# Performance work log

Measured on AMD Instinct MI355X. Metric: run time of the kernel, lower is better.

The kernel has to match this reference:

```python
import jax, jax.numpy as jnp
import numpy as np


def _lstm_layer(x, W, U, b):
    """Keras-style LSTM (gate order i,f,c,o). x: (B,T,F). Returns (hs: (B,T,H), h_last: (B,H))."""
    B, T, F = x.shape
    H = U.shape[0]
    # Precompute input projections for all timesteps: (T, B, 4H)
    zx = jnp.einsum('btf,fk->tbk', x, W) + b

    def step(carry, zx_t):
        h, c = carry
        z = zx_t + h @ U  # (B, 4H)
        i, f, g, o = jnp.split(z, 4, axis=-1)
        i = jax.nn.sigmoid(i)
        f = jax.nn.sigmoid(f)
        g = jnp.tanh(g)
        o = jax.nn.sigmoid(o)
        c = f * c + i * g
        h = o * jnp.tanh(c)
        return (h, c), h

    h0 = jnp.zeros((B, H), dtype=x.dtype)
    c0 = jnp.zeros((B, H), dtype=x.dtype)
    (h_last, _), hs = jax.lax.scan(step, (h0, c0), zx)
    return jnp.transpose(hs, (1, 0, 2)), h_last


def setup_inputs() -> dict:
    key = jax.random.key(0)
    ks = jax.random.split(key, 8)
    B, T, F, H, L = 512, 128, 64, 1024, 1
    s = 0.05
    return {
        'x': jax.random.normal(ks[0], (B, T, F), dtype=jnp.float32),
        'W1': jax.random.normal(ks[1], (F, 4 * H), dtype=jnp.float32) * s,
        'U1': jax.random.normal(ks[2], (H, 4 * H), dtype=jnp.float32) * s,
        'b1': jnp.zeros((4 * H,), dtype=jnp.float32),
        'W2': jax.random.normal(ks[3], (H, 4 * H), dtype=jnp.float32) * s,
        'U2': jax.random.normal(ks[4], (H, 4 * H), dtype=jnp.float32) * s,
        'b2': jnp.zeros((4 * H,), dtype=jnp.float32),
        'Wd': jax.random.normal(ks[5], (H, L), dtype=jnp.float32) * s,
        'bd': jnp.zeros((L,), dtype=jnp.float32),
    }


def reference(x, W1, U1, b1, W2, U2, b2, Wd, bd):
    # Layer 1: return_sequences=True (dropout inactive at inference)
    h1_seq, _ = _lstm_layer(x, W1, U1, b1)
    # Layer 2: return_sequences=False -> last hidden state
    _, h2_last = _lstm_layer(h1_seq, W2, U2, b2)
    # Dense sigmoid head
    return jax.nn.sigmoid(h2_last @ Wd + bd)
```

## Files before the change

kernel.cpp:

```cpp
#include <hip/hip_runtime.h>
#include <hip/hip_bf16.h>
#include <cstdint>


typedef __attribute__((ext_vector_type(8))) _Float16 half8;
typedef __attribute__((ext_vector_type(4))) float    float4v;

__device__ __forceinline__ float sigf(float x) { return 1.0f / (1.0f + __expf(-x)); }
__device__ __forceinline__ float tanhfast(float x) { return 2.0f * sigf(2.0f * x) - 1.0f; }

static constexpr size_t HPS = 32ull * 32 * 512;

struct FragSet {
    half8 A[4];
    half8 B[4][2];
};

__global__ __launch_bounds__(512, 2) void fused_step(
    int s,
    const _Float16* __restrict__ xp,
    const _Float16* __restrict__ P1,
    const _Float16* __restrict__ P2,
    const float* __restrict__ b1, float* __restrict__ c1, _Float16* __restrict__ h1p,
    const float* __restrict__ b2, float* __restrict__ c2, _Float16* __restrict__ h2p)
{
    const int b    = blockIdx.x;
    const int role = (b >> 3) & 1;
    const int tile = ((b >> 4) << 3) | (b & 7);

    const _Float16 *As0, *As1, *Pk;
    const float* bias; float* cs; _Float16* hop;
    int KC0, KCB, KCT;
    if (role == 0) {
        const int t = s; if (t >= 128) return;
        As0 = xp + (size_t)t * 32768;  KC0 = 2;
        As1 = h1p + (size_t)(t & 1) * HPS;
        Pk = P1; KCB = 34; KCT = 34;
        bias = b1; cs = c1;
        hop = h1p + (size_t)(1 - (t & 1)) * HPS;
    } else {
        const int t = s - 1; if (t < 0) return;
        As0 = h1p + (size_t)(1 - (t & 1)) * HPS; KC0 = 32;
        As1 = h2p + (size_t)(t & 1) * HPS;
        Pk = P2; KCB = 64; KCT = 64;
        bias = b2; cs = c2;
        hop = h2p + (size_t)(1 - (t & 1)) * HPS;
    }

    const int tid = threadIdx.x;
    const int w   = tid >> 6;
    const int l   = tid & 63;
    const int q   = l >> 4;
    const int c16 = l & 15;
    const int mh  = w & 1;
    const int kp  = w >> 1;

    const int m0  = (tile >> 5) * 128;
    const int n0  = (tile & 31) * 32;
    const int mG0 = (m0 >> 4) + mh * 4;

    const size_t l8 = (size_t)l * 8;

    const _Float16* bp[4][2];
#pragma unroll
    for (int g = 0; g < 4; ++g)
#pragma unroll
        for (int nf = 0; nf < 2; ++nf)
            bp[g][nf] = Pk + ((size_t)(g * 64 + (n0 >> 4) + nf) * KCB) * 512 + l8;

    float4v acc[4][4][2] = {};

    auto loadS = [&](int kc, FragSet& S) {
        const _Float16* ab; size_t astr;
        if (kc < KC0) { ab = As0 + (size_t)kc * 512;         astr = (size_t)KC0 * 512; }
        else          { ab = As1 + (size_t)(kc - KC0) * 512; astr = 32ull * 512; }
        ab += (size_t)mG0 * astr + l8;
#pragma unroll
        for (int ms = 0; ms < 4; ++ms)
            S.A[ms] = *(const half8*)(ab + (size_t)ms * astr);
#pragma unroll
        for (int g = 0; g < 4; ++g)
#pragma unroll
            for (int nf = 0; nf < 2; ++nf)
                S.B[g][nf] = *(const half8*)(bp[g][nf] + (size_t)kc * 512);
    };
    auto computeS = [&](const FragSet& S) {
#pragma unroll
        for (int g = 0; g < 4; ++g)
#pragma unroll
            for (int ms = 0; ms < 4; ++ms)
#pragma unroll
                for (int nf = 0; nf < 2; ++nf)
                    acc[g][ms][nf] = __builtin_amdgcn_mfma_f32_16x16x32_f16(
                        S.A[ms], S.B[g][nf], acc[g][ms][nf], 0, 0, 0);
    };

    const int base = KCT >> 2;
    const int rem  = KCT & 3;
    const int len  = base + (kp < rem ? 1 : 0);
    const int kcS  = kp * base + (kp < rem ? kp : rem);

    FragSet S;
#pragma unroll 2
    for (int kc = kcS; kc < kcS + len; ++kc) {
        loadS(kc, S);
        computeS(S);
    }

    __shared__ float4v red[8][16][64];
    if ((kp & 1) == 0) {
#pragma unroll
        for (int g = 0; g < 4; ++g)
#pragma unroll
            for (int ms = 0; ms < 4; ++ms)
                red[w][g * 4 + ms][l] = acc[g][ms][1];
    } else {
#pragma unroll
        for (int g = 0; g < 4; ++g)
#pragma unroll
            for (int ms = 0; ms < 4; ++ms)
                red[w][g * 4 + ms][l] = acc[g][ms][0];
    }
    __syncthreads();
    float4v acc1[4][4];
    if ((kp & 1) == 0) {
#pragma unroll
        for (int g = 0; g < 4; ++g)
#pragma unroll
            for (int ms = 0; ms < 4; ++ms)
                acc1[g][ms] = acc[g][ms][0] + red[w ^ 2][g * 4 + ms][l];
    } else {
#pragma unroll
        for (int g = 0; g < 4; ++g)
#pragma unroll
            for (int ms = 0; ms < 4; ++ms)
                acc1[g][ms] = acc[g][ms][1] + red[w ^ 2][g * 4 + ms][l];
    }
    __syncthreads();
    if ((kp >> 1) == 0) {
#pragma unroll
        for (int g = 0; g < 4; ++g)
#pragma unroll
            for (int j = 0; j < 2; ++j)
                red[w][g * 2 + j][l] = acc1[g][2 + j];
    } else {
#pragma unroll
        for (int g = 0; g < 4; ++g)
#pragma unroll
            for (int j = 0; j < 2; ++j)
                red[w][g * 2 + j][l] = acc1[g][j];
    }
    __syncthreads();
    float4v out[4][2];
    if ((kp >> 1) == 0) {
#pragma unroll
        for (int g = 0; g < 4; ++g)
#pragma unroll
            for (int j = 0; j < 2; ++j)
                out[g][j] = acc1[g][j] + red[w ^ 4][g * 2 + j][l];
    } else {
#pragma unroll
        for (int g = 0; g < 4; ++g)
#pragma unroll
            for (int j = 0; j < 2; ++j)
                out[g][j] = acc1[g][2 + j] + red[w ^ 4][g * 2 + j][l];
    }

    const int own_nf  = kp & 1;
    const int own_msp = kp >> 1;
    const int ng = n0 + own_nf * 16 + c16;
    const float bi  = bias[ng];
    const float bff = bias[1024 + ng];
    const float bg  = bias[2048 + ng];
    const float bo  = bias[3072 + ng];
    const int kcH   = n0 >> 5;
    const int laneW = (own_nf * 2 + (c16 >> 3)) << 4;
    const int jW    = c16 & 7;
    float4v* cfrag = (float4v*)cs;
    const size_t cbase = ((size_t)tile * 8 + w) * 2;
#pragma unroll
    for (int j = 0; j < 2; ++j) {
        const int msg = own_msp * 2 + j;
        const int mG  = mG0 + msg;
        _Float16* hg = hop + ((size_t)(mG * 32 + kcH)) * 512 + (size_t)laneW * 8 + jW;
        float4v cold = cfrag[(cbase + j) * 64 + l];
        float4v cnew;
#pragma unroll
        for (int i = 0; i < 4; ++i) {
            const float zi = out[0][j][i] + bi;
            const float zf = out[1][j][i] + bff;
            const float zg = out[2][j][i] + bg;
            const float zo = out[3][j][i] + bo;
            const float ig = sigf(zi);
            const float fg = sigf(zf);
            const float gg = tanhfast(zg);
            const float og = sigf(zo);
            const float cc = fg * cold[i] + ig * gg;
            cnew[i] = cc;
            hg[(q * 4 + i) * 8] = (_Float16)(og * tanhfast(cc));
        }
        cfrag[(cbase + j) * 64 + l] = cnew;
    }
}

__global__ void pack_weights(const float* __restrict__ W, const float* __restrict__ U,
                             int KA, int KC, _Float16* __restrict__ out)
{
    const size_t e = (size_t)blockIdx.x * blockDim.x + threadIdx.x;
    const size_t total = (size_t)256 * KC * 512;
    if (e >= total) return;
    const int j    = (int)(e & 7);
    const int lane = (int)((e >> 3) & 63);
    const size_t g = e >> 9;
    const int kc  = (int)(g % KC);
    const int ntG = (int)(g / KC);
    const int col = ntG * 16 + (lane & 15);
    const int k   = kc * 32 + (lane >> 4) * 8 + j;
    const float v = (k < KA) ? W[(size_t)k * 4096 + col]
                             : U[(size_t)(k - KA) * 4096 + col];
    out[e] = (_Float16)v;
}

__global__ void pack_x(const float* __restrict__ x, _Float16* __restrict__ xp)
{
    const int e = blockIdx.x * blockDim.x + threadIdx.x;
    if (e >= 512 * 128 * 64) return;
    const int j  = e & 7;
    const int l  = (e >> 3) & 63;
    const int g  = e >> 9;
    const int kc = g & 1;
    const int tm = g >> 1;
    const int mG = tm & 31;
    const int t  = tm >> 5;
    const int m  = mG * 16 + (l & 15);
    const int f  = kc * 32 + (l >> 4) * 8 + j;
    xp[e] = (_Float16)x[((size_t)m * 128 + t) * 64 + f];
}

__global__ __launch_bounds__(64) void dense_head(const _Float16* __restrict__ h2p,
                                                 const float* __restrict__ Wd,
                                                 const float* __restrict__ bd,
                                                 float* __restrict__ out)
{
    const int mG = blockIdx.x;
    const int l  = threadIdx.x;
    float s = 0.0f;
    for (int kc = 0; kc < 32; ++kc) {
        half8 f = *(const half8*)(h2p + ((size_t)(mG * 32 + kc)) * 512 + (size_t)l * 8);
        const int kb = kc * 32 + (l >> 4) * 8;
#pragma unroll
        for (int j = 0; j < 8; ++j) s += (float)f[j] * Wd[kb + j];
    }
    s += __shfl_xor(s, 16);
    s += __shfl_xor(s, 32);
    if (l < 16) out[mG * 16 + l] = 1.0f / (1.0f + __expf(-(s + bd[0])));
}


extern "C" void kernel_launch(void* const* d_in, const int* in_sizes, int n_in,
                              void* d_out, int out_size, void* d_ws, size_t ws_size,
                              hipStream_t stream)
{
    const float* x  = (const float*)d_in[0];
    const float* W1 = (const float*)d_in[1];
    const float* U1 = (const float*)d_in[2];
    const float* b1 = (const float*)d_in[3];
    const float* W2 = (const float*)d_in[4];
    const float* U2 = (const float*)d_in[5];
    const float* b2 = (const float*)d_in[6];
    const float* Wd = (const float*)d_in[7];
    const float* bd = (const float*)d_in[8];
    float* out = (float*)d_out;

    char* ws = (char*)d_ws;
    size_t off = 0;
    auto alloc = [&](size_t bytes) {
        char* p = ws + off;
        off = (off + bytes + 255) & ~(size_t)255;
        return p;
    };
    _Float16* xp  = (_Float16*)alloc(512ull * 128 * 64 * 2);
    _Float16* P1  = (_Float16*)alloc(256ull * 34 * 512 * 2);
    _Float16* P2  = (_Float16*)alloc(256ull * 64 * 512 * 2);
    _Float16* h1p = (_Float16*)alloc(2ull * HPS * 2);
    _Float16* h2p = (_Float16*)alloc(2ull * HPS * 2);
    float*    c1  = (float*)alloc(512ull * 1024 * 4);
    float*    c2  = (float*)alloc(512ull * 1024 * 4);

    hipMemsetAsync(c1, 0, 512ull * 1024 * 4, stream);
    hipMemsetAsync(c2, 0, 512ull * 1024 * 4, stream);
    hipMemsetAsync(h1p, 0, HPS * 2, stream);
    hipMemsetAsync(h2p, 0, HPS * 2, stream);

    pack_x<<<(512 * 128 * 64 + 255) / 256, 256, 0, stream>>>(x, xp);
    pack_weights<<<(256 * 34 * 512 + 255) / 256, 256, 0, stream>>>(W1, U1, 64, 34, P1);
    pack_weights<<<(256 * 64 * 512 + 255) / 256, 256, 0, stream>>>(W2, U2, 1024, 64, P2);

    for (int s = 0; s <= 128; ++s) {
        fused_step<<<256, 512, 0, stream>>>(s, xp, P1, P2,
                                            b1, c1, h1p, b2, c2, h2p);
    }
    dense_head<<<32, 64, 0, stream>>>(h2p, Wd, bd, out);
}
```

Baseline: 3.053 ms.

## Balance work by letting layer-1 blocks compute part of layer-2 K-reduction

Layer-1 blocks (34 K-chunks) finish their own GEMM and then compute the last 16 of layer 2's 64 K-chunks for the same tile. They write partial sums to a global scratch buffer and raise a per-tile flag. Layer-2 blocks handle the remaining 48 chunks, spin-wait on the flag, add the partials, and run the epilogue. This evens out the per-block critical path between the two roles. In exchange it adds a global round-trip for the partials and an inter-block spin-wait that assumes both blocks are co-resident.

```diff
diff --git a/kernel.cpp b/kernel.cpp
--- a/kernel.cpp
+++ b/kernel.cpp
@@ -22,30 +22,12 @@
     const _Float16* __restrict__ P1,
     const _Float16* __restrict__ P2,
     const float* __restrict__ b1, float* __restrict__ c1, _Float16* __restrict__ h1p,
-    const float* __restrict__ b2, float* __restrict__ c2, _Float16* __restrict__ h2p)
+    const float* __restrict__ b2, float* __restrict__ c2, _Float16* __restrict__ h2p,
+    float* __restrict__ pscr, int* __restrict__ flags)
 {
     const int b    = blockIdx.x;
     const int role = (b >> 3) & 1;
     const int tile = ((b >> 4) << 3) | (b & 7);
-
-    const _Float16 *As0, *As1, *Pk;
-    const float* bias; float* cs; _Float16* hop;
-    int KC0, KCB, KCT;
-    if (role == 0) {
-        const int t = s; if (t >= 128) return;
-        As0 = xp + (size_t)t * 32768;  KC0 = 2;
-        As1 = h1p + (size_t)(t & 1) * HPS;
-        Pk = P1; KCB = 34; KCT = 34;
-        bias = b1; cs = c1;
-        hop = h1p + (size_t)(1 - (t & 1)) * HPS;
-    } else {
-        const int t = s - 1; if (t < 0) return;
-        As0 = h1p + (size_t)(1 - (t & 1)) * HPS; KC0 = 32;
-        As1 = h2p + (size_t)(t & 1) * HPS;
-        Pk = P2; KCB = 64; KCT = 64;
-        bias = b2; cs = c2;
-        hop = h2p + (size_t)(1 - (t & 1)) * HPS;
-    }
 
     const int tid = threadIdx.x;
     const int w   = tid >> 6;
@@ -58,148 +40,207 @@
     const int m0  = (tile >> 5) * 128;
     const int n0  = (tile & 31) * 32;
     const int mG0 = (m0 >> 4) + mh * 4;
-
     const size_t l8 = (size_t)l * 8;
 
-    const _Float16* bp[4][2];
-#pragma unroll
-    for (int g = 0; g < 4; ++g)
-#pragma unroll
-        for (int nf = 0; nf < 2; ++nf)
-            bp[g][nf] = Pk + ((size_t)(g * 64 + (n0 >> 4) + nf) * KCB) * 512 + l8;
-
-    float4v acc[4][4][2] = {};
-
-    auto loadS = [&](int kc, FragSet& S) {
-        const _Float16* ab; size_t astr;
-        if (kc < KC0) { ab = As0 + (size_t)kc * 512;         astr = (size_t)KC0 * 512; }
-        else          { ab = As1 + (size_t)(kc - KC0) * 512; astr = 32ull * 512; }
-        ab += (size_t)mG0 * astr + l8;
-#pragma unroll
-        for (int ms = 0; ms < 4; ++ms)
-            S.A[ms] = *(const half8*)(ab + (size_t)ms * astr);
+    __shared__ float4v red[8][16][64];
+
+    auto run_phase = [&](const _Float16* Pk, int KCB,
+                         const _Float16* As0, const _Float16* As1, int KC0,
+                         int kcS, int len, float4v (&o)[4][2]) {
+        const _Float16* bp[4][2];
 #pragma unroll
         for (int g = 0; g < 4; ++g)
 #pragma unroll
             for (int nf = 0; nf < 2; ++nf)
-                S.B[g][nf] = *(const half8*)(bp[g][nf] + (size_t)kc * 512);
+                bp[g][nf] = Pk + ((size_t)(g * 64 + (n0 >> 4) + nf) * KCB) * 512 + l8;
+
+        float4v acc[4][4][2] = {};
+        FragSet S;
+#pragma unroll 2
+        for (int kc = kcS; kc < kcS + len; ++kc) {
+            const _Float16* ab; size_t astr;
+            if (kc < KC0) { ab = As0 + (size_t)kc * 512;         astr = (size_t)KC0 * 512; }
+            else          { ab = As1 + (size_t)(kc - KC0) * 512; astr = 32ull * 512; }
+            ab += (size_t)mG0 * astr + l8;
+#pragma unroll
+            for (int ms = 0; ms < 4; ++ms)
+                S.A[ms] = *(const half8*)(ab + (size_t)ms * astr);
+#pragma unroll
+            for (int g = 0; g < 4; ++g)
+#pragma unroll
+                for (int nf = 0; nf < 2; ++nf)
+                    S.B[g][nf] = *(const half8*)(bp[g][nf] + (size_t)kc * 512);
+#pragma unroll
+            for (int g = 0; g < 4; ++g)
+#pragma unroll
+                for (int ms = 0; ms < 4; ++ms)
+#pragma unroll
+                    for (int nf = 0; nf < 2; ++nf)
+                        acc[g][ms][nf] = __builtin_amdgcn_mfma_f32_16x16x32_f16(
+                            S.A[ms], S.B[g][nf], acc[g][ms][nf], 0, 0, 0);
+        }
+
+        if ((kp & 1) == 0) {
+#pragma unroll
+            for (int g = 0; g < 4; ++g)
+#pragma unroll
+                for (int ms = 0; ms < 4; ++ms)
+                    red[w][g * 4 + ms][l] = acc[g][ms][1];
+        } else {
+#pragma unroll
+            for (int g = 0; g < 4; ++g)
+#pragma unroll
+                for (int ms = 0; ms < 4; ++ms)
+                    red[w][g * 4 + ms][l] = acc[g][ms][0];
+        }
+        __syncthreads();
+        float4v acc1[4][4];
+        if ((kp & 1) == 0) {
+#pragma unroll
+            for (int g = 0; g < 4; ++g)
+#pragma unroll
+                for (int ms = 0; ms < 4; ++ms)
+                    acc1[g][ms] = acc[g][ms][0] + red[w ^ 2][g * 4 + ms][l];
+        } else {
+#pragma unroll
+            for (int g = 0; g < 4; ++g)
+#pragma unroll
+                for (int ms = 0; ms < 4; ++ms)
+                    acc1[g][ms] = acc[g][ms][1] + red[w ^ 2][g * 4 + ms][l];
+        }
+        __syncthreads();
+        if ((kp >> 1) == 0) {
+#pragma unroll
+            for (int g = 0; g < 4; ++g)
+#pragma unroll
+                for (int j = 0; j < 2; ++j)
+                    red[w][g * 2 + j][l] = acc1[g][2 + j];
+        } else {
+#pragma unroll
+            for (int g = 0; g < 4; ++g)
+#pragma unroll
+                for (int j = 0; j < 2; ++j)
+                    red[w][g * 2 + j][l] = acc1[g][j];
+        }
+        __syncthreads();
+        if ((kp >> 1) == 0) {
+#pragma unroll
+            for (int g = 0; g < 4; ++g)
+#pragma unroll
+                for (int j = 0; j < 2; ++j)
+                    o[g][j] = acc1[g][j] + red[w ^ 4][g * 2 + j][l];
+        } else {
+#pragma unroll
+            for (int g = 0; g < 4; ++g)
+#pragma unroll
+                for (int j = 0; j < 2; ++j)
+                    o[g][j] = acc1[g][2 + j] + red[w ^ 4][g * 2 + j][l];
+        }
     };
-    auto computeS = [&](const FragSet& S) {
-#pragma unroll
-        for (int g = 0; g < 4; ++g)
-#pragma unroll
-            for (int ms = 0; ms < 4; ++ms)
-#pragma unroll
-                for (int nf = 0; nf < 2; ++nf)
-                    acc[g][ms][nf] = __builtin_amdgcn_mfma_f32_16x16x32_f16(
-                        S.A[ms], S.B[g][nf], acc[g][ms][nf], 0, 0, 0);
+
+    auto epilogue = [&](const float4v (&o)[4][2], const float* bias,
+                        float* cs, _Float16* hop) {
+        const int own_nf  = kp & 1;
+        const int own_msp = kp >> 1;
+        const int ng = n0 + own_nf * 16 + c16;
+        const float bi  = bias[ng];
+        const float bff = bias[1024 + ng];
+        const float bg  = bias[2048 + ng];
+        const float bo  = bias[3072 + ng];
+        const int kcH   = n0 >> 5;
+        const int laneW = (own_nf * 2 + (c16 >> 3)) << 4;
+        const int jW    = c16 & 7;
+        float4v* cfrag = (float4v*)cs;
+        const size_t cbase = ((size_t)tile * 8 + w) * 2;
+#pragma unroll
+        for (int j = 0; j < 2; ++j) {
+            const int msg = own_msp * 2 + j;
+            const int mG  = mG0 + msg;
+            _Float16* hg = hop + ((size_t)(mG * 32 + kcH)) * 512
+                         + (size_t)laneW * 8 + jW;
+            float4v cold = cfrag[(cbase + j) * 64 + l];
+            float4v cnew;
+#pragma unroll
+            for (int i = 0; i < 4; ++i) {
+                const float zi = o[0][j][i] + bi;
+                const float zf = o[1][j][i] + bff;
+                const float zg = o[2][j][i] + bg;
+                const float zo = o[3][j][i] + bo;
+                const float ig = sigf(zi);
+                const float fg = sigf(zf);
+                const float gg = tanhfast(zg);
+                const float og = sigf(zo);
+                const float cc = fg * cold[i] + ig * gg;
+                cnew[i] = cc;
+                hg[(q * 4 + i) * 8] = (_Float16)(og * tanhfast(cc));
+            }
+            cfrag[(cbase + j) * 64 + l] = cnew;
+        }
     };
 
-    const int base = KCT >> 2;
-    const int rem  = KCT & 3;
-    const int len  = base + (kp < rem ? 1 : 0);
-    const int kcS  = kp * base + (kp < rem ? kp : rem);
-
-    FragSet S;
-#pragma unroll 2
-    for (int kc = kcS; kc < kcS + len; ++kc) {
-        loadS(kc, S);
-        computeS(S);
-    }
-
-    __shared__ float4v red[8][16][64];
-    if ((kp & 1) == 0) {
-#pragma unroll
-        for (int g = 0; g < 4; ++g)
-#pragma unroll
-            for (int ms = 0; ms < 4; ++ms)
-                red[w][g * 4 + ms][l] = acc[g][ms][1];
+    if (role == 0) {
+        if (s >= 128) return;
+        const int t = s;
+        {
+            const _Float16* As0 = xp + (size_t)t * 32768;
+            const _Float16* As1 = h1p + (size_t)(t & 1) * HPS;
+            _Float16* hop = h1p + (size_t)(1 - (t & 1)) * HPS;
+            const int len = 8 + (kp < 2 ? 1 : 0);
+            const int kcS = kp * 8 + (kp < 2 ? kp : 2);
+            float4v out[4][2];
+            run_phase(P1, 34, As0, As1, 2, kcS, len, out);
+            epilogue(out, b1, c1, hop);
+        }
+        if (s >= 1) {
+            __syncthreads();
+            const int t2 = s - 1;
+            const _Float16* A20 = h1p + (size_t)(1 - (t2 & 1)) * HPS;
+            const _Float16* A21 = h2p + (size_t)(t2 & 1) * HPS;
+            float4v out2[4][2];
+            run_phase(P2, 64, A20, A21, 32, 48 + kp * 4, 4, out2);
+            float4v* ps = (float4v*)pscr;
+            const size_t pb = ((size_t)tile * 8 + w) * 2;
+#pragma unroll
+            for (int j = 0; j < 2; ++j)
+#pragma unroll
+                for (int g = 0; g < 4; ++g)
+                    ps[((pb + j) * 4 + g) * 64 + l] = out2[g][j];
+            __threadfence();
+            __syncthreads();
+            if (tid == 0) *(volatile int*)(flags + tile) = s;
+        }
     } else {
-#pragma unroll
-        for (int g = 0; g < 4; ++g)
-#pragma unroll
-            for (int ms = 0; ms < 4; ++ms)
-                red[w][g * 4 + ms][l] = acc[g][ms][0];
-    }
-    __syncthreads();
-    float4v acc1[4][4];
-    if ((kp & 1) == 0) {
-#pragma unroll
-        for (int g = 0; g < 4; ++g)
-#pragma unroll
-            for (int ms = 0; ms < 4; ++ms)
-                acc1[g][ms] = acc[g][ms][0] + red[w ^ 2][g * 4 + ms][l];
-    } else {
-#pragma unroll
-        for (int g = 0; g < 4; ++g)
-#pragma unroll
-            for (int ms = 0; ms < 4; ++ms)
-                acc1[g][ms] = acc[g][ms][1] + red[w ^ 2][g * 4 + ms][l];
-    }
-    __syncthreads();
-    if ((kp >> 1) == 0) {
-#pragma unroll
-        for (int g = 0; g < 4; ++g)
+        if (s < 1) return;
+        const int t = s - 1;
+        const bool helped = (s < 128);
+        const _Float16* As0 = h1p + (size_t)(1 - (t & 1)) * HPS;
+        const _Float16* As1 = h2p + (size_t)(t & 1) * HPS;
+        _Float16* hop = h2p + (size_t)(1 - (t & 1)) * HPS;
+        const int lim = helped ? 12 : 16;
+        float4v out[4][2];
+        run_phase(P2, 64, As0, As1, 32, kp * lim, lim, out);
+        if (helped) {
+            if (tid == 0) {
+                volatile int* vf = flags + tile;
+                while (*vf != s) {}
+            }
+            __syncthreads();
+            __threadfence();
+            const float4v* ps = (const float4v*)pscr;
+            const size_t pb = ((size_t)tile * 8 + w) * 2;
 #pragma unroll
             for (int j = 0; j < 2; ++j)
-                red[w][g * 2 + j][l] = acc1[g][2 + j];
-    } else {
-#pragma unroll
-        for (int g = 0; g < 4; ++g)
-#pragma unroll
-            for (int j = 0; j < 2; ++j)
-                red[w][g * 2 + j][l] = acc1[g][j];
-    }
-    __syncthreads();
-    float4v out[4][2];
-    if ((kp >> 1) == 0) {
-#pragma unroll
-        for (int g = 0; g < 4; ++g)
-#pragma unroll
-            for (int j = 0; j < 2; ++j)
-                out[g][j] = acc1[g][j] + red[w ^ 4][g * 2 + j][l];
-    } else {
-#pragma unroll
-        for (int g = 0; g < 4; ++g)
-#pragma unroll
-            for (int j = 0; j < 2; ++j)
-                out[g][j] = acc1[g][2 + j] + red[w ^ 4][g * 2 + j][l];
-    }
-
-    const int own_nf  = kp & 1;
-    const int own_msp = kp >> 1;
-    const int ng = n0 + own_nf * 16 + c16;
-    const float bi  = bias[ng];
-    const float bff = bias[1024 + ng];
-    const float bg  = bias[2048 + ng];
-    const float bo  = bias[3072 + ng];
-    const int kcH   = n0 >> 5;
-    const int laneW = (own_nf * 2 + (c16 >> 3)) << 4;
-    const int jW    = c16 & 7;
-    float4v* cfrag = (float4v*)cs;
-    const size_t cbase = ((size_t)tile * 8 + w) * 2;
-#pragma unroll
-    for (int j = 0; j < 2; ++j) {
-        const int msg = own_msp * 2 + j;
-        const int mG  = mG0 + msg;
-        _Float16* hg = hop + ((size_t)(mG * 32 + kcH)) * 512 + (size_t)laneW * 8 + jW;
-        float4v cold = cfrag[(cbase + j) * 64 + l];
-        float4v cnew;
-#pragma unroll
-        for (int i = 0; i < 4; ++i) {
-            const float zi = out[0][j][i] + bi;
-            const float zf = out[1][j][i] + bff;
-            const float zg = out[2][j][i] + bg;
-            const float zo = out[3][j][i] + bo;
-            const float ig = sigf(zi);
-            const float fg = sigf(zf);
-            const float gg = tanhfast(zg);
-            const float og = sigf(zo);
-            const float cc = fg * cold[i] + ig * gg;
-            cnew[i] = cc;
-            hg[(q * 4 + i) * 8] = (_Float16)(og * tanhfast(cc));
-        }
-        cfrag[(cbase + j) * 64 + l] = cnew;
+#pragma unroll
+                for (int g = 0; g < 4; ++g) {
+                    const volatile float* pv =
+                        (const volatile float*)&ps[((pb + j) * 4 + g) * 64 + l];
+                    out[g][j][0] += pv[0];
+                    out[g][j][1] += pv[1];
+                    out[g][j][2] += pv[2];
+                    out[g][j][3] += pv[3];
+                }
+        }
+        epilogue(out, b2, c2, hop);
     }
 }
 
@@ -286,6 +327,8 @@
     _Float16* h2p = (_Float16*)alloc(2ull * HPS * 2);
     float*    c1  = (float*)alloc(512ull * 1024 * 4);
     float*    c2  = (float*)alloc(512ull * 1024 * 4);
+    float*    pscr  = (float*)alloc(8ull << 20);
+    int*      flags = (int*)alloc(128 * 4);
 
     hipMemsetAsync(c1, 0, 512ull * 1024 * 4, stream);
     hipMemsetAsync(c2, 0, 512ull * 1024 * 4, stream);
@@ -298,7 +341,8 @@
 
     for (int s = 0; s <= 128; ++s) {
         fused_step<<<256, 512, 0, stream>>>(s, xp, P1, P2,
-                                            b1, c1, h1p, b2, c2, h2p);
+                                            b1, c1, h1p, b2, c2, h2p,
+                                            pscr, flags);
     }
     dense_head<<<32, 64, 0, stream>>>(h2p, Wd, bd, out);
 }
```

After: 9.960 ms. +226.3%, slower.
